# Kernel optimization log

Measured on AMD Instinct MI355X. Metric: run time of the kernel, lower is better.

Reference implementation:

```python
import jax, jax.numpy as jnp
import numpy as np

D_MODEL = 1024
H = 16
D_H = D_MODEL // H
B = 8
S = 1024
NEG_INF = -1e9


def setup_inputs() -> dict:
    key = jax.random.key(0)
    ks = jax.random.split(key, 8)
    Qs = jax.random.normal(ks[0], (B, S, D_MODEL), dtype=jnp.float32)
    Ks = jax.random.normal(ks[1], (B, S, D_MODEL), dtype=jnp.float32)
    Vs = jax.random.normal(ks[2], (B, S, D_MODEL), dtype=jnp.float32)
    mask_3d = jnp.zeros((B, S, S), dtype=bool)
    # Parameters: torch.rand -> uniform[0,1) for per-head projections
    W_Q = jax.random.uniform(ks[3], (H, D_MODEL, D_H), dtype=jnp.float32)
    W_K = jax.random.uniform(ks[4], (H, D_MODEL, D_H), dtype=jnp.float32)
    W_V = jax.random.uniform(ks[5], (H, D_MODEL, D_H), dtype=jnp.float32)
    # Output nn.Linear(h*d_h, d_model): weight [d_model, h*d_h], bias [d_model]
    lim = 1.0 / np.sqrt(H * D_H)
    W_out = jax.random.uniform(ks[6], (D_MODEL, H * D_H), minval=-lim, maxval=lim, dtype=jnp.float32)
    b_out = jax.random.uniform(ks[7], (D_MODEL,), minval=-lim, maxval=lim, dtype=jnp.float32)
    return {"Qs": Qs, "Ks": Ks, "Vs": Vs, "mask_3d": mask_3d,
            "W_Q": W_Q, "W_K": W_K, "W_V": W_V, "W_out": W_out, "b_out": b_out}


def reference(Qs, Ks, Vs, mask_3d, W_Q, W_K, W_V, W_out, b_out):
    # Fused per-head projections: avoid the explicit repeat in the torch code.
    q = jnp.einsum('bsk,hkl->bhsl', Qs, W_Q)  # [B,H,S,D_H]
    k = jnp.einsum('bsk,hkl->bhsl', Ks, W_K)
    v = jnp.einsum('bsk,hkl->bhsl', Vs, W_V)
    scale = 1.0 / jnp.sqrt(jnp.asarray(D_H, dtype=q.dtype))
    scores = jnp.einsum('bhqd,bhkd->bhqk', q, k) * scale  # [B,H,S,S]
    scores = jnp.where(mask_3d[:, None, :, :], NEG_INF, scores)
    attn = jax.nn.softmax(scores, axis=-1)
    out = jnp.einsum('bhqk,bhkd->bhqd', attn, v)  # [B,H,S,D_H]
    # chunk along head-batch dim then cat along feature dim == head-major concat
    out = jnp.transpose(out, (0, 2, 1, 3)).reshape(B, S, H * D_H)
    return out @ W_out.T + b_out
```

## Files before the change

### kernel.cpp

```cpp
#include <hip/hip_runtime.h>

#define DM 1024
#define H_ 16
#define DH 64
#define B_ 8
#define S_ 1024

typedef _Float16 half8 __attribute__((ext_vector_type(8)));
typedef _Float16 half4 __attribute__((ext_vector_type(4)));
typedef __fp16 fp16x2 __attribute__((ext_vector_type(2)));
typedef float f32x4 __attribute__((ext_vector_type(4)));
typedef float f32x16 __attribute__((ext_vector_type(16)));
typedef unsigned int uint;

static __device__ __forceinline__ uint pkrtz(float a, float b) {
    fp16x2 h = __builtin_amdgcn_cvt_pkrtz(a, b);
    return __builtin_bit_cast(uint, h);
}
#define PSWAP(d, s) asm volatile("v_permlane32_swap_b32 %0, %1" : "+v"(d), "+v"(s))

static __device__ __forceinline__ void gload16(const _Float16* g, _Float16* l) {
    __builtin_amdgcn_global_load_lds(
        (const __attribute__((address_space(1))) unsigned int*)(const void*)g,
        (__attribute__((address_space(3))) unsigned int*)(void*)l,
        16, 0, 0);
}

__global__ __launch_bounds__(256) void packw_k(
    const float* __restrict__ WQ, const float* __restrict__ WK,
    const float* __restrict__ WV,
    _Float16* __restrict__ wqh, _Float16* __restrict__ wql,
    _Float16* __restrict__ wkh, _Float16* __restrict__ wkl,
    _Float16* __restrict__ wv)
{
    __shared__ __align__(16) _Float16 Lh[64][72];
    __shared__ __align__(16) _Float16 Ll[64][72];
    const int t = threadIdx.x;
    const int kb = blockIdx.x;
    const int h  = blockIdx.y;

    #pragma unroll
    for (int s = 0; s < 3; ++s) {
        const float* W = (s == 0) ? WQ : ((s == 1) ? WK : WV);
        const int krow = t >> 2, lc = t & 3;
        const float* rp = W + (((size_t)h * 1024 + kb * 64 + krow) * 64 + lc * 16);
        #pragma unroll
        for (int q4 = 0; q4 < 4; ++q4) {
            float4 f = ((const float4*)rp)[q4];
            float vv0 = f.x, vv1 = f.y, vv2 = f.z, vv3 = f.w;
            int l0 = lc * 16 + q4 * 4;
            _Float16 h0 = (_Float16)vv0; Lh[l0 + 0][krow] = h0; Ll[l0 + 0][krow] = (_Float16)(vv0 - (float)h0);
            _Float16 h1 = (_Float16)vv1; Lh[l0 + 1][krow] = h1; Ll[l0 + 1][krow] = (_Float16)(vv1 - (float)h1);
            _Float16 h2 = (_Float16)vv2; Lh[l0 + 2][krow] = h2; Ll[l0 + 2][krow] = (_Float16)(vv2 - (float)h2);
            _Float16 h3 = (_Float16)vv3; Lh[l0 + 3][krow] = h3; Ll[l0 + 3][krow] = (_Float16)(vv3 - (float)h3);
        }
        __syncthreads();
        const int l = t >> 2, pc = t & 3;
        #pragma unroll
        for (int hp = 0; hp < 2; ++hp) {
            int p = pc + 4 * hp;
            int lc2 = p ^ (l & 7);
            half8 vh = *(const half8*)&Lh[l][lc2 * 8];
            half8 vl = *(const half8*)&Ll[l][lc2 * 8];
            size_t off = (size_t)(h * 64 + l) * DM + kb * 64 + p * 8;
            if (s == 0) { *(half8*)(wqh + off) = vh; *(half8*)(wql + off) = vl; }
            else if (s == 1) { *(half8*)(wkh + off) = vh; *(half8*)(wkl + off) = vl; }
            else { *(half8*)(wv + off) = vh; }
        }
        __syncthreads();
    }
}

__global__ __launch_bounds__(256) void packo_k(
    const float* __restrict__ WO, _Float16* __restrict__ wo)
{
    int idx8 = blockIdx.x * 256 + threadIdx.x;
    int n = idx8 >> 7;
    int c = idx8 & 127;
    int p = (c & ~7) | ((c & 7) ^ (n & 7));
    const float* rp = WO + ((size_t)n * DM + c * 8);
    float4 a = ((const float4*)rp)[0];
    float4 b = ((const float4*)rp)[1];
    half8 v;
    v[0] = (_Float16)a.x; v[1] = (_Float16)a.y; v[2] = (_Float16)a.z; v[3] = (_Float16)a.w;
    v[4] = (_Float16)b.x; v[5] = (_Float16)b.y; v[6] = (_Float16)b.z; v[7] = (_Float16)b.w;
    *(half8*)(wo + (size_t)n * DM + p * 8) = v;
}

__global__ __launch_bounds__(256) void scan_k(
    const unsigned char* __restrict__ mask, unsigned char* __restrict__ scan)
{
    __shared__ int s_red[4];
    const int t = threadIdx.x;
    const int q64 = blockIdx.x, k64 = blockIdx.y, b = blockIdx.z;
    uint4 mv = *(const uint4*)(mask + ((size_t)b * S_ + q64 * 64 + (t >> 2)) * S_ + k64 * 64 + (t & 3) * 16);
    int a = (mv.x | mv.y | mv.z | mv.w) != 0;
    unsigned long long bal = __ballot(a);
    if ((t & 63) == 0) s_red[t >> 6] = (bal != 0ull);
    __syncthreads();
    if (t == 0)
        scan[(b * 16 + q64) * 16 + k64] =
            (unsigned char)(s_red[0] | s_red[1] | s_red[2] | s_red[3]);
}

__global__ __launch_bounds__(512) void gemm_split_k(
    const float* __restrict__ A0, const float* __restrict__ A1,
    const _Float16* __restrict__ Bh0, const _Float16* __restrict__ Bl0,
    const _Float16* __restrict__ Bh1, const _Float16* __restrict__ Bl1,
    _Float16* __restrict__ Chi0, _Float16* __restrict__ Clo0,
    _Float16* __restrict__ Chi1, _Float16* __restrict__ Clo1)
{
    const int lid = blockIdx.x + 8 * blockIdx.y + 512 * blockIdx.z;
    const int xcd = lid & 7, k2 = lid >> 3;
    const int G = xcd * 16 + (k2 >> 3);
    const int bxv = k2 & 7, byv = G & 63, z = G >> 6;

    const float* A = z ? A1 : A0;
    const _Float16* Bh = z ? Bh1 : Bh0;
    const _Float16* Bl = z ? Bl1 : Bl0;
    _Float16* Chi = z ? Chi1 : Chi0;
    _Float16* Clo = z ? Clo1 : Clo0;

    __shared__ __align__(16) _Float16 SM[32768];
    _Float16* Ah  = SM;
    _Float16* Al  = SM + 8192;
    _Float16* Bhs = SM + 16384;
    _Float16* Bls = SM + 24576;

    const int t = threadIdx.x;
    const int lane = t & 63;
    const int w = t >> 6;
    const int wm = (w >> 1) * 32;
    const int wn = (w & 1) * 64;
    const int l15 = lane & 15;
    const int l4g = lane >> 4;

    const int bm = byv * 128;
    const int bn = bxv * 128;

    f32x4 acc[2][4] = {};

    float4 ar[4];
    auto aload = [&](int KT) {
        #pragma unroll
        for (int i = 0; i < 4; ++i)
            ar[i] = *(const float4*)(A + (size_t)(bm + (t >> 4) + 32 * i) * DM + KT * 64 + (t & 15) * 4);
    };
    auto awr = [&]() {
        #pragma unroll
        for (int i = 0; i < 4; ++i) {
            int row = (t >> 4) + 32 * i;
            int c4 = t & 15;
            float4 v = ar[i];
            half4 hv, lv;
            hv[0] = (_Float16)v.x; lv[0] = (_Float16)(v.x - (float)hv[0]);
            hv[1] = (_Float16)v.y; lv[1] = (_Float16)(v.y - (float)hv[1]);
            hv[2] = (_Float16)v.z; lv[2] = (_Float16)(v.z - (float)hv[2]);
            hv[3] = (_Float16)v.w; lv[3] = (_Float16)(v.w - (float)hv[3]);
            int off = row * 64 + (((c4 >> 1) ^ (row & 7)) * 8) + (c4 & 1) * 4;
            *(half4*)&Ah[off] = hv;
            *(half4*)&Al[off] = lv;
        }
    };
    auto bgl = [&](int KT) {
        #pragma unroll
        for (int j = 0; j < 2; ++j) {
            int rr = w * 16 + j * 8 + (lane >> 3);
            const size_t so = (size_t)(bn + rr) * DM + KT * 64 + (lane & 7) * 8;
            gload16(Bh + so, &Bhs[(w * 16 + j * 8) * 64]);
            gload16(Bl + so, &Bls[(w * 16 + j * 8) * 64]);
        }
    };

    aload(0);
    bgl(0);
    for (int kt = 0; kt < 16; ++kt) {
        awr();
        __syncthreads();
        if (kt < 15) aload(kt + 1);
        #pragma unroll
        for (int ks = 0; ks < 2; ++ks) {
            half8 ah[2], al[2], bh[4], bl[4];
            const int slotx = (ks * 4 + l4g);
            #pragma unroll
            for (int mi = 0; mi < 2; ++mi) {
                int r = wm + mi * 16 + l15;
                int off = r * 64 + (slotx ^ (l15 & 7)) * 8;
                ah[mi] = *(const half8*)&Ah[off];
                al[mi] = *(const half8*)&Al[off];
            }
            #pragma unroll
            for (int ni = 0; ni < 4; ++ni) {
                int r = wn + ni * 16 + l15;
                int off = r * 64 + (slotx ^ (l15 & 7)) * 8;
                bh[ni] = *(const half8*)&Bhs[off];
                bl[ni] = *(const half8*)&Bls[off];
            }
            #pragma unroll
            for (int mi = 0; mi < 2; ++mi)
                #pragma unroll
                for (int ni = 0; ni < 4; ++ni) {
                    acc[mi][ni] = __builtin_amdgcn_mfma_f32_16x16x32_f16(ah[mi], bh[ni], acc[mi][ni], 0, 0, 0);
                    acc[mi][ni] = __builtin_amdgcn_mfma_f32_16x16x32_f16(ah[mi], bl[ni], acc[mi][ni], 0, 0, 0);
                    acc[mi][ni] = __builtin_amdgcn_mfma_f32_16x16x32_f16(al[mi], bh[ni], acc[mi][ni], 0, 0, 0);
                }
        }
        __syncthreads();
        if (kt < 15) bgl(kt + 1);
    }

    #pragma unroll
    for (int mi = 0; mi < 2; ++mi)
        #pragma unroll
        for (int ni = 0; ni < 4; ++ni) {
            int col = bn + wn + ni * 16 + l15;
            #pragma unroll
            for (int r = 0; r < 4; ++r) {
                int row = bm + wm + mi * 16 + l4g * 4 + r;
                float val = acc[mi][ni][r];
                _Float16 hv = (_Float16)val;
                Chi[(size_t)row * DM + col] = hv;
                Clo[(size_t)row * DM + col] = (_Float16)(val - (float)hv);
            }
        }
}

__global__ __launch_bounds__(256) void gemm_v_k(
    const float* __restrict__ A, const _Float16* __restrict__ Bt,
    _Float16* __restrict__ C)
{
    const int lid = blockIdx.x + 8 * blockIdx.y;
    const int xcd = lid & 7, k2 = lid >> 3;
    const int G = xcd * 8 + (k2 >> 3);
    const int bxv = k2 & 7, byv = G;

    __shared__ __align__(16) _Float16 SM[25600];
    _Float16* As  = SM;
    _Float16* Bsb = SM + 9216;

    const int t = threadIdx.x;
    const int lane = t & 63;
    const int w = t >> 6;
    const int wm = (w >> 1) * 64;
    const int wn = (w & 1) * 64;
    const int l15 = lane & 15;
    const int l4g = lane >> 4;

    const int bm = byv * 128;
    const int bn = bxv * 128;

    f32x4 acc[4][4] = {};

    const int arow = t >> 4, ac4 = t & 15;
    float4 ar[8];
    auto aload = [&](int KT) {
        #pragma unroll
        for (int i = 0; i < 8; ++i)
            ar[i] = *(const float4*)(A + (size_t)(bm + arow + 16 * i) * DM + KT * 64 + ac4 * 4);
    };
    auto awr = [&]() {
        #pragma unroll
        for (int i = 0; i < 8; ++i) {
            float4 v = ar[i];
            half4 hv;
            hv[0] = (_Float16)v.x; hv[1] = (_Float16)v.y;
            hv[2] = (_Float16)v.z; hv[3] = (_Float16)v.w;
            *(half4*)&As[(arow + 16 * i) * 72 + ac4 * 4] = hv;
        }
    };
    auto bgl = [&](int KT, int buf) {
        _Float16* Bd = Bsb + buf * 8192;
        #pragma unroll
        for (int j = 0; j < 4; ++j) {
            int rr = w * 32 + j * 8 + (lane >> 3);
            gload16(Bt + (size_t)(bn + rr) * DM + KT * 64 + (lane & 7) * 8,
                    &Bd[(w * 32 + j * 8) * 64]);
        }
    };

    aload(0);
    bgl(0, 0);
    for (int kt = 0; kt < 16; ++kt) {
        const _Float16* Bcur = Bsb + (kt & 1) * 8192;
        awr();
        __syncthreads();
        if (kt < 15) { aload(kt + 1); bgl(kt + 1, (kt + 1) & 1); }
        #pragma unroll
        for (int ks = 0; ks < 2; ++ks) {
            half8 a[4], b[4];
            #pragma unroll
            for (int mi = 0; mi < 4; ++mi)
                a[mi] = *(const half8*)&As[(wm + mi * 16 + l15) * 72 + ks * 32 + l4g * 8];
            #pragma unroll
            for (int ni = 0; ni < 4; ++ni) {
                int row = wn + ni * 16 + l15;
                int slot = (ks * 4 + l4g) ^ (l15 & 7);
                b[ni] = *(const half8*)&Bcur[row * 64 + slot * 8];
            }
            #pragma unroll
            for (int mi = 0; mi < 4; ++mi)
                #pragma unroll
                for (int ni = 0; ni < 4; ++ni)
                    acc[mi][ni] = __builtin_amdgcn_mfma_f32_16x16x32_f16(a[mi], b[ni], acc[mi][ni], 0, 0, 0);
        }
        __syncthreads();
    }

    _Float16* Tw = SM + w * 4608;
    #pragma unroll
    for (int mi = 0; mi < 4; ++mi)
        #pragma unroll
        for (int ni = 0; ni < 4; ++ni)
            #pragma unroll
            for (int r = 0; r < 4; ++r)
                Tw[(ni * 16 + l15) * 72 + mi * 16 + l4g * 4 + r] = (_Float16)acc[mi][ni][r];
    __syncthreads();
    {
        const int mg0 = bm + wm;
        const int b = mg0 >> 10, s0 = mg0 & 1023;
        _Float16* op = C + ((size_t)b * DM + (bn + wn + lane)) * S_ + s0;
        #pragma unroll
        for (int c8 = 0; c8 < 8; ++c8)
            *(half8*)(op + c8 * 8) = *(const half8*)&Tw[lane * 72 + c8 * 8];
    }
}

__global__ __launch_bounds__(256) void gemm_out_k(
    const _Float16* __restrict__ A, const _Float16* __restrict__ Bt,
    float* __restrict__ C, const float* __restrict__ bias)
{
    const int lid = blockIdx.x + 8 * blockIdx.y;
    const int xcd = lid & 7, k2 = lid >> 3;
    const int G = xcd * 8 + (k2 >> 3);
    const int bxv = k2 & 7, byv = G;

    __shared__ __align__(16) _Float16 SM[25600];
    _Float16* As  = SM;
    _Float16* Bsb = SM + 9216;

    const int t = threadIdx.x;
    const int lane = t & 63;
    const int w = t >> 6;
    const int wm = (w >> 1) * 64;
    const int wn = (w & 1) * 64;
    const int l15 = lane & 15;
    const int l4g = lane >> 4;

    const int bm = byv * 128;
    const int bn = bxv * 128;

    f32x4 acc[4][4] = {};

    uint4 arr[4];
    auto aload = [&](int KT) {
        #pragma unroll
        for (int i = 0; i < 4; ++i)
            arr[i] = *(const uint4*)(A + (size_t)(bm + (t >> 3) + 32 * i) * DM + KT * 64 + (t & 7) * 8);
    };
    auto awr = [&]() {
        #pragma unroll
        for (int i = 0; i < 4; ++i)
            *(uint4*)&As[((t >> 3) + 32 * i) * 72 + (t & 7) * 8] = arr[i];
    };
    auto bgl = [&](int KT, int buf) {
        _Float16* Bd = Bsb + buf * 8192;
        #pragma unroll
        for (int j = 0; j < 4; ++j) {
            int rr = w * 32 + j * 8 + (lane >> 3);
            gload16(Bt + (size_t)(bn + rr) * DM + KT * 64 + (lane & 7) * 8,
                    &Bd[(w * 32 + j * 8) * 64]);
        }
    };

    aload(0);
    bgl(0, 0);
    for (int kt = 0; kt < 16; ++kt) {
        const _Float16* Bcur = Bsb + (kt & 1) * 8192;
        awr();
        __syncthreads();
        if (kt < 15) { aload(kt + 1); bgl(kt + 1, (kt + 1) & 1); }
        #pragma unroll
        for (int ks = 0; ks < 2; ++ks) {
            half8 a[4], b[4];
            #pragma unroll
            for (int mi = 0; mi < 4; ++mi)
                a[mi] = *(const half8*)&As[(wm + mi * 16 + l15) * 72 + ks * 32 + l4g * 8];
            #pragma unroll
            for (int ni = 0; ni < 4; ++ni) {
                int row = wn + ni * 16 + l15;
                int slot = (ks * 4 + l4g) ^ (l15 & 7);
                b[ni] = *(const half8*)&Bcur[row * 64 + slot * 8];
            }
            #pragma unroll
            for (int mi = 0; mi < 4; ++mi)
                #pragma unroll
                for (int ni = 0; ni < 4; ++ni)
                    acc[mi][ni] = __builtin_amdgcn_mfma_f32_16x16x32_f16(a[mi], b[ni], acc[mi][ni], 0, 0, 0);
        }
        __syncthreads();
    }

    #pragma unroll
    for (int mi = 0; mi < 4; ++mi)
        #pragma unroll
        for (int ni = 0; ni < 4; ++ni) {
            int col = bn + wn + ni * 16 + l15;
            #pragma unroll
            for (int r = 0; r < 4; ++r) {
                int row = bm + wm + mi * 16 + l4g * 4 + r;
                C[(size_t)row * DM + col] = acc[mi][ni][r] + bias[col];
            }
        }
}

__global__ __launch_bounds__(256) void attn_k(
    const _Float16* __restrict__ qhg, const _Float16* __restrict__ qlg,
    const _Float16* __restrict__ khg, const _Float16* __restrict__ klg,
    const _Float16* __restrict__ vtg, const unsigned char* __restrict__ maskg,
    const unsigned char* __restrict__ scanp, _Float16* __restrict__ ho)
{
    __shared__ __align__(16) _Float16 Kh[64][72];
    __shared__ __align__(16) _Float16 Kl[64][72];
    __shared__ __align__(16) _Float16 Vt[64][72];

    const int t = threadIdx.x;
    const int lane = t & 63;
    const int w = t >> 6;
    const int l31 = lane & 31;
    const int hi = lane >> 5;

    const int j = blockIdx.y + 16 * blockIdx.z;
    const int head = 16 * blockIdx.x + (j >> 3);
    const int qt = j & 7;
    const int h = head & 15;
    const int b = head >> 4;

    const int colbase = h * DH;
    const int qrow = qt * 128 + w * 32 + l31;

    half8 qfh[4], qfl[4];
    {
        const size_t base = ((size_t)b * S_ + qrow) * DM + colbase;
        #pragma unroll
        for (int ds = 0; ds < 4; ++ds) {
            qfh[ds] = *(const half8*)(qhg + base + ds * 16 + hi * 8);
            qfl[ds] = *(const half8*)(qlg + base + ds * 16 + hi * 8);
        }
    }

    float m_q = -1e30f, ls = 0.0f;
    f32x16 accO0 = {};
    f32x16 accO1 = {};

    const int r0 = t >> 3;
    const int c0 = (t & 7) * 8;
    const _Float16* kph = khg + ((size_t)b * S_) * DM + colbase;
    const _Float16* kpl = klg + ((size_t)b * S_) * DM + colbase;
    const _Float16* vp  = vtg + ((size_t)b * DM + colbase) * S_;
    const unsigned char* sc0 = scanp + (b * 16 + 2 * qt) * 16;
    const unsigned char* sc1 = scanp + (b * 16 + 2 * qt + 1) * 16;

    uint4 akh0, akh1, akl0, akl1, av0, av1;
#define ALOAD(KT) do { \
        akh0 = *(const uint4*)(kph + (size_t)((KT) * 64 + r0) * DM + c0);       \
        akh1 = *(const uint4*)(kph + (size_t)((KT) * 64 + 32 + r0) * DM + c0);  \
        akl0 = *(const uint4*)(kpl + (size_t)((KT) * 64 + r0) * DM + c0);       \
        akl1 = *(const uint4*)(kpl + (size_t)((KT) * 64 + 32 + r0) * DM + c0);  \
        av0  = *(const uint4*)(vp + (size_t)r0 * S_ + (KT) * 64 + c0);          \
        av1  = *(const uint4*)(vp + (size_t)(32 + r0) * S_ + (KT) * 64 + c0);   \
    } while (0)
#define AWRITE() do { \
        *(uint4*)&Kh[r0][c0] = akh0; *(uint4*)&Kh[32 + r0][c0] = akh1; \
        *(uint4*)&Kl[r0][c0] = akl0; *(uint4*)&Kl[32 + r0][c0] = akl1; \
        *(uint4*)&Vt[r0][c0] = av0;  *(uint4*)&Vt[32 + r0][c0] = av1;  \
    } while (0)

    ALOAD(0);
    AWRITE();
    int msk = sc0[0] | sc1[0];

    const float SC = 0.125f * 1.44269504089f;
    const float THRRAW = 8.0f / SC;

    for (int kt = 0; kt < 16; ++kt) {
        __syncthreads();
        const int mskcur = msk;
        if (kt < 15) {
            ALOAD(kt + 1);
            msk = sc0[kt + 1] | sc1[kt + 1];
        }

        f32x16 sa0 = {}, sa1 = {};
        __builtin_amdgcn_s_setprio(1);
        #pragma unroll
        for (int ds = 0; ds < 4; ++ds) {
            half8 kh0 = *(const half8*)&Kh[l31][ds * 16 + hi * 8];
            half8 kl0 = *(const half8*)&Kl[l31][ds * 16 + hi * 8];
            half8 kh1 = *(const half8*)&Kh[32 + l31][ds * 16 + hi * 8];
            half8 kl1 = *(const half8*)&Kl[32 + l31][ds * 16 + hi * 8];
            sa0 = __builtin_amdgcn_mfma_f32_32x32x16_f16(kh0, qfh[ds], sa0, 0, 0, 0);
            sa0 = __builtin_amdgcn_mfma_f32_32x32x16_f16(kh0, qfl[ds], sa0, 0, 0, 0);
            sa0 = __builtin_amdgcn_mfma_f32_32x32x16_f16(kl0, qfh[ds], sa0, 0, 0, 0);
            sa1 = __builtin_amdgcn_mfma_f32_32x32x16_f16(kh1, qfh[ds], sa1, 0, 0, 0);
            sa1 = __builtin_amdgcn_mfma_f32_32x32x16_f16(kh1, qfl[ds], sa1, 0, 0, 0);
            sa1 = __builtin_amdgcn_mfma_f32_32x32x16_f16(kl1, qfh[ds], sa1, 0, 0, 0);
        }
        __builtin_amdgcn_s_setprio(0);

        if (mskcur) {
            const unsigned char* mrow = maskg + ((size_t)b * S_ + qrow) * S_ + kt * 64;
            #pragma unroll
            for (int e = 0; e < 16; ++e) {
                int kl_ = (e & 3) + 8 * (e >> 2) + 4 * hi;
                if (mrow[kl_]) sa0[e] = -1e9f;
                if (mrow[32 + kl_]) sa1[e] = -1e9f;
            }
        }

        float rm = sa0[0];
        #pragma unroll
        for (int e = 1; e < 16; ++e) rm = fmaxf(rm, sa0[e]);
        #pragma unroll
        for (int e = 0; e < 16; ++e) rm = fmaxf(rm, sa1[e]);
        rm = fmaxf(rm, __shfl_xor(rm, 32));
        if (__any(rm > m_q + THRRAW)) {
            const float mn = fmaxf(m_q, rm);
            const float sfac = exp2f((m_q - mn) * SC);
            m_q = mn;
            ls *= sfac;
            #pragma unroll
            for (int e = 0; e < 16; ++e) { accO0[e] *= sfac; accO1[e] *= sfac; }
        }
        const float nmn = -m_q * SC;
        float rs = 0.0f;
        #pragma unroll
        for (int e = 0; e < 16; ++e) { sa0[e] = exp2f(fmaf(sa0[e], SC, nmn)); rs += sa0[e]; }
        #pragma unroll
        for (int e = 0; e < 16; ++e) { sa1[e] = exp2f(fmaf(sa1[e], SC, nmn)); rs += sa1[e]; }
        rs += __shfl_xor(rs, 32);
        ls += rs;

        half8 pf[4];
        {
            uint c0_ = pkrtz(sa0[0], sa0[1]),  c1_ = pkrtz(sa0[2], sa0[3]);
            uint c2_ = pkrtz(sa0[4], sa0[5]),  c3_ = pkrtz(sa0[6], sa0[7]);
            uint c4_ = pkrtz(sa0[8], sa0[9]),  c5_ = pkrtz(sa0[10], sa0[11]);
            uint c6_ = pkrtz(sa0[12], sa0[13]), c7_ = pkrtz(sa0[14], sa0[15]);
            PSWAP(c0_, c2_); PSWAP(c1_, c3_);
            PSWAP(c4_, c6_); PSWAP(c5_, c7_);
            uint4 u0 = {c0_, c1_, c2_, c3_}, u1 = {c4_, c5_, c6_, c7_};
            pf[0] = __builtin_bit_cast(half8, u0);
            pf[1] = __builtin_bit_cast(half8, u1);
        }
        {
            uint c0_ = pkrtz(sa1[0], sa1[1]),  c1_ = pkrtz(sa1[2], sa1[3]);
            uint c2_ = pkrtz(sa1[4], sa1[5]),  c3_ = pkrtz(sa1[6], sa1[7]);
            uint c4_ = pkrtz(sa1[8], sa1[9]),  c5_ = pkrtz(sa1[10], sa1[11]);
            uint c6_ = pkrtz(sa1[12], sa1[13]), c7_ = pkrtz(sa1[14], sa1[15]);
            PSWAP(c0_, c2_); PSWAP(c1_, c3_);
            PSWAP(c4_, c6_); PSWAP(c5_, c7_);
            uint4 u0 = {c0_, c1_, c2_, c3_}, u1 = {c4_, c5_, c6_, c7_};
            pf[2] = __builtin_bit_cast(half8, u0);
            pf[3] = __builtin_bit_cast(half8, u1);
        }
        __builtin_amdgcn_s_setprio(1);
        #pragma unroll
        for (int kc = 0; kc < 4; ++kc) {
            half8 vf0 = *(const half8*)&Vt[l31][kc * 16 + hi * 8];
            half8 vf1 = *(const half8*)&Vt[32 + l31][kc * 16 + hi * 8];
            accO0 = __builtin_amdgcn_mfma_f32_32x32x16_f16(vf0, pf[kc], accO0, 0, 0, 0);
            accO1 = __builtin_amdgcn_mfma_f32_32x32x16_f16(vf1, pf[kc], accO1, 0, 0, 0);
        }
        __builtin_amdgcn_s_setprio(0);

        __syncthreads();
        if (kt < 15) AWRITE();
    }
#undef ALOAD
#undef AWRITE

    const float inv = 1.0f / ls;
    _Float16* orow = ho + ((size_t)b * S_ + qrow) * DM + colbase;
    #pragma unroll
    for (int g2 = 0; g2 < 4; ++g2) {
        half4 hv0, hv1;
        #pragma unroll
        for (int e = 0; e < 4; ++e) {
            hv0[e] = (_Float16)(accO0[g2 * 4 + e] * inv);
            hv1[e] = (_Float16)(accO1[g2 * 4 + e] * inv);
        }
        *(half4*)(orow + g2 * 8 + hi * 4) = hv0;
        *(half4*)(orow + 32 + g2 * 8 + hi * 4) = hv1;
    }
}

extern "C" void kernel_launch(void* const* d_in, const int* in_sizes, int n_in,
                              void* d_out, int out_size, void* d_ws, size_t ws_size,
                              hipStream_t stream)
{
    const float* Qs = (const float*)d_in[0];
    const float* Ks = (const float*)d_in[1];
    const float* Vs = (const float*)d_in[2];
    const unsigned char* mask = (const unsigned char*)d_in[3];
    const float* WQ = (const float*)d_in[4];
    const float* WK = (const float*)d_in[5];
    const float* WV = (const float*)d_in[6];
    const float* WO = (const float*)d_in[7];
    const float* bo = (const float*)d_in[8];

    char* ws = (char*)d_ws;
    const size_t MB = 1024 * 1024;
    _Float16* wqh = (_Float16*)(ws + 0 * MB);
    _Float16* wql = (_Float16*)(ws + 2 * MB);
    _Float16* wkh = (_Float16*)(ws + 4 * MB);
    _Float16* wkl = (_Float16*)(ws + 6 * MB);
    _Float16* wv  = (_Float16*)(ws + 8 * MB);
    _Float16* wo  = (_Float16*)(ws + 10 * MB);
    _Float16* qhi = (_Float16*)(ws + 12 * MB);
    _Float16* qlo = (_Float16*)(ws + 28 * MB);
    _Float16* khi = (_Float16*)(ws + 44 * MB);
    _Float16* klo = (_Float16*)(ws + 60 * MB);
    _Float16* vt  = (_Float16*)(ws + 76 * MB);
    _Float16* hh  = (_Float16*)(ws + 92 * MB);
    unsigned char* scan = (unsigned char*)(ws + 108 * MB);

    packw_k<<<dim3(16, 16), 256, 0, stream>>>(WQ, WK, WV, wqh, wql, wkh, wkl, wv);
    packo_k<<<512, 256, 0, stream>>>(WO, wo);
    scan_k<<<dim3(16, 16, 8), 256, 0, stream>>>(mask, scan);

    gemm_split_k<<<dim3(8, 64, 2), 512, 0, stream>>>(
        Qs, Ks, wqh, wql, wkh, wkl, qhi, qlo, khi, klo);

    gemm_v_k<<<dim3(8, 64), 256, 0, stream>>>(Vs, wv, vt);

    attn_k<<<dim3(8, 16, 8), 256, 0, stream>>>(qhi, qlo, khi, klo, vt, mask, scan, hh);

    gemm_out_k<<<dim3(8, 64), 256, 0, stream>>>(hh, wo, (float*)d_out, bo);
}
```

Measured before the change: 305.7 us.

## Load GEMM A operands directly into MFMA registers and double-buffer B tiles

In the three projection and output GEMMs, the A operand is now read straight from global memory into registers in MFMA fragment layout. This drops the LDS staging step, the fp16 split done at LDS-write time, and one barrier per k-step. The B tile becomes double-buffered in LDS so the next tile's async load overlaps the current MFMAs. gemm_v and gemm_out move to 512 threads with smaller per-wave tiles. The cost is uncoalesced per-lane A reads (32-byte chunks per row) and more register pressure for the prefetched fp32 fragments.

Result: slower. 374.9 us (+22.6%).

```diff
diff --git a/kernel.cpp b/kernel.cpp
--- a/kernel.cpp
+++ b/kernel.cpp
@@ -24,6 +24,17 @@
         (const __attribute__((address_space(1))) unsigned int*)(const void*)g,
         (__attribute__((address_space(3))) unsigned int*)(void*)l,
         16, 0, 0);
+}
+
+static __device__ __forceinline__ void cvt8(float4 a, float4 b, half8& hv, half8& lv) {
+    hv[0] = (_Float16)a.x; lv[0] = (_Float16)(a.x - (float)hv[0]);
+    hv[1] = (_Float16)a.y; lv[1] = (_Float16)(a.y - (float)hv[1]);
+    hv[2] = (_Float16)a.z; lv[2] = (_Float16)(a.z - (float)hv[2]);
+    hv[3] = (_Float16)a.w; lv[3] = (_Float16)(a.w - (float)hv[3]);
+    hv[4] = (_Float16)b.x; lv[4] = (_Float16)(b.x - (float)hv[4]);
+    hv[5] = (_Float16)b.y; lv[5] = (_Float16)(b.y - (float)hv[5]);
+    hv[6] = (_Float16)b.z; lv[6] = (_Float16)(b.z - (float)hv[6]);
+    hv[7] = (_Float16)b.w; lv[7] = (_Float16)(b.w - (float)hv[7]);
 }
 
 __global__ __launch_bounds__(256) void packw_k(
@@ -122,10 +133,6 @@
     _Float16* Clo = z ? Clo1 : Clo0;
 
     __shared__ __align__(16) _Float16 SM[32768];
-    _Float16* Ah  = SM;
-    _Float16* Al  = SM + 8192;
-    _Float16* Bhs = SM + 16384;
-    _Float16* Bls = SM + 24576;
 
     const int t = threadIdx.x;
     const int lane = t & 63;
@@ -140,73 +147,62 @@
 
     f32x4 acc[2][4] = {};
 
-    float4 ar[4];
+    const float* aptr = A + (size_t)(bm + wm + l15) * DM + l4g * 8;
+    float4 arf[8];
     auto aload = [&](int KT) {
         #pragma unroll
-        for (int i = 0; i < 4; ++i)
-            ar[i] = *(const float4*)(A + (size_t)(bm + (t >> 4) + 32 * i) * DM + KT * 64 + (t & 15) * 4);
-    };
-    auto awr = [&]() {
-        #pragma unroll
-        for (int i = 0; i < 4; ++i) {
-            int row = (t >> 4) + 32 * i;
-            int c4 = t & 15;
-            float4 v = ar[i];
-            half4 hv, lv;
-            hv[0] = (_Float16)v.x; lv[0] = (_Float16)(v.x - (float)hv[0]);
-            hv[1] = (_Float16)v.y; lv[1] = (_Float16)(v.y - (float)hv[1]);
-            hv[2] = (_Float16)v.z; lv[2] = (_Float16)(v.z - (float)hv[2]);
-            hv[3] = (_Float16)v.w; lv[3] = (_Float16)(v.w - (float)hv[3]);
-            int off = row * 64 + (((c4 >> 1) ^ (row & 7)) * 8) + (c4 & 1) * 4;
-            *(half4*)&Ah[off] = hv;
-            *(half4*)&Al[off] = lv;
-        }
-    };
-    auto bgl = [&](int KT) {
-        #pragma unroll
-        for (int j = 0; j < 2; ++j) {
-            int rr = w * 16 + j * 8 + (lane >> 3);
+        for (int mi = 0; mi < 2; ++mi)
+            #pragma unroll
+            for (int ks = 0; ks < 2; ++ks) {
+                const float* p = aptr + (size_t)mi * 16 * DM + KT * 64 + ks * 32;
+                arf[(mi * 2 + ks) * 2 + 0] = *(const float4*)p;
+                arf[(mi * 2 + ks) * 2 + 1] = *(const float4*)(p + 4);
+            }
+    };
+    half8 ahf[4], alf[4];
+    auto acvt = [&]() {
+        #pragma unroll
+        for (int f = 0; f < 4; ++f)
+            cvt8(arf[f * 2], arf[f * 2 + 1], ahf[f], alf[f]);
+    };
+    auto bgl = [&](int KT, int buf) {
+        _Float16* Bhd = SM + buf * 16384;
+        _Float16* Bld = Bhd + 8192;
+        #pragma unroll
+        for (int jj = 0; jj < 2; ++jj) {
+            int rr = w * 16 + jj * 8 + (lane >> 3);
             const size_t so = (size_t)(bn + rr) * DM + KT * 64 + (lane & 7) * 8;
-            gload16(Bh + so, &Bhs[(w * 16 + j * 8) * 64]);
-            gload16(Bl + so, &Bls[(w * 16 + j * 8) * 64]);
+            gload16(Bh + so, Bhd + (w * 16 + jj * 8) * 64);
+            gload16(Bl + so, Bld + (w * 16 + jj * 8) * 64);
         }
     };
 
     aload(0);
-    bgl(0);
+    bgl(0, 0);
+    __syncthreads();
     for (int kt = 0; kt < 16; ++kt) {
-        awr();
+        acvt();
+        if (kt < 15) { aload(kt + 1); bgl(kt + 1, (kt + 1) & 1); }
+        const _Float16* Bhc = SM + (kt & 1) * 16384;
+        const _Float16* Blc = Bhc + 8192;
+        #pragma unroll
+        for (int ks = 0; ks < 2; ++ks) {
+            const int slotx = ks * 4 + l4g;
+            #pragma unroll
+            for (int ni = 0; ni < 4; ++ni) {
+                int off = (wn + ni * 16 + l15) * 64 + ((slotx ^ (l15 & 7)) * 8);
+                half8 bh = *(const half8*)&Bhc[off];
+                half8 bl = *(const half8*)&Blc[off];
+                #pragma unroll
+                for (int mi = 0; mi < 2; ++mi) {
+                    const int f = mi * 2 + ks;
+                    acc[mi][ni] = __builtin_amdgcn_mfma_f32_16x16x32_f16(ahf[f], bh, acc[mi][ni], 0, 0, 0);
+                    acc[mi][ni] = __builtin_amdgcn_mfma_f32_16x16x32_f16(ahf[f], bl, acc[mi][ni], 0, 0, 0);
+                    acc[mi][ni] = __builtin_amdgcn_mfma_f32_16x16x32_f16(alf[f], bh, acc[mi][ni], 0, 0, 0);
+                }
+            }
+        }
         __syncthreads();
-        if (kt < 15) aload(kt + 1);
-        #pragma unroll
-        for (int ks = 0; ks < 2; ++ks) {
-            half8 ah[2], al[2], bh[4], bl[4];
-            const int slotx = (ks * 4 + l4g);
-            #pragma unroll
-            for (int mi = 0; mi < 2; ++mi) {
-                int r = wm + mi * 16 + l15;
-                int off = r * 64 + (slotx ^ (l15 & 7)) * 8;
-                ah[mi] = *(const half8*)&Ah[off];
-                al[mi] = *(const half8*)&Al[off];
-            }
-            #pragma unroll
-            for (int ni = 0; ni < 4; ++ni) {
-                int r = wn + ni * 16 + l15;
-                int off = r * 64 + (slotx ^ (l15 & 7)) * 8;
-                bh[ni] = *(const half8*)&Bhs[off];
-                bl[ni] = *(const half8*)&Bls[off];
-            }
-            #pragma unroll
-            for (int mi = 0; mi < 2; ++mi)
-                #pragma unroll
-                for (int ni = 0; ni < 4; ++ni) {
-                    acc[mi][ni] = __builtin_amdgcn_mfma_f32_16x16x32_f16(ah[mi], bh[ni], acc[mi][ni], 0, 0, 0);
-                    acc[mi][ni] = __builtin_amdgcn_mfma_f32_16x16x32_f16(ah[mi], bl[ni], acc[mi][ni], 0, 0, 0);
-                    acc[mi][ni] = __builtin_amdgcn_mfma_f32_16x16x32_f16(al[mi], bh[ni], acc[mi][ni], 0, 0, 0);
-                }
-        }
-        __syncthreads();
-        if (kt < 15) bgl(kt + 1);
     }
 
     #pragma unroll
@@ -225,7 +221,7 @@
         }
 }
 
-__global__ __launch_bounds__(256) void gemm_v_k(
+__global__ __launch_bounds__(512) void gemm_v_k(
     const float* __restrict__ A, const _Float16* __restrict__ Bt,
     _Float16* __restrict__ C)
 {
@@ -234,14 +230,12 @@
     const int G = xcd * 8 + (k2 >> 3);
     const int bxv = k2 & 7, byv = G;
 
-    __shared__ __align__(16) _Float16 SM[25600];
-    _Float16* As  = SM;
-    _Float16* Bsb = SM + 9216;
+    __shared__ __align__(16) _Float16 SM[18432];
 
     const int t = threadIdx.x;
     const int lane = t & 63;
     const int w = t >> 6;
-    const int wm = (w >> 1) * 64;
+    const int wm = (w >> 1) * 32;
     const int wn = (w & 1) * 64;
     const int l15 = lane & 15;
     const int l4g = lane >> 4;
@@ -249,83 +243,84 @@
     const int bm = byv * 128;
     const int bn = bxv * 128;
 
-    f32x4 acc[4][4] = {};
-
-    const int arow = t >> 4, ac4 = t & 15;
-    float4 ar[8];
+    f32x4 acc[2][4] = {};
+
+    const float* aptr = A + (size_t)(bm + wm + l15) * DM + l4g * 8;
+    float4 arf[8];
     auto aload = [&](int KT) {
         #pragma unroll
-        for (int i = 0; i < 8; ++i)
-            ar[i] = *(const float4*)(A + (size_t)(bm + arow + 16 * i) * DM + KT * 64 + ac4 * 4);
-    };
-    auto awr = [&]() {
-        #pragma unroll
-        for (int i = 0; i < 8; ++i) {
-            float4 v = ar[i];
-            half4 hv;
-            hv[0] = (_Float16)v.x; hv[1] = (_Float16)v.y;
-            hv[2] = (_Float16)v.z; hv[3] = (_Float16)v.w;
-            *(half4*)&As[(arow + 16 * i) * 72 + ac4 * 4] = hv;
+        for (int mi = 0; mi < 2; ++mi)
+            #pragma unroll
+            for (int ks = 0; ks < 2; ++ks) {
+                const float* p = aptr + (size_t)mi * 16 * DM + KT * 64 + ks * 32;
+                arf[(mi * 2 + ks) * 2 + 0] = *(const float4*)p;
+                arf[(mi * 2 + ks) * 2 + 1] = *(const float4*)(p + 4);
+            }
+    };
+    half8 ahf[4];
+    auto acvt = [&]() {
+        #pragma unroll
+        for (int f = 0; f < 4; ++f) {
+            float4 a = arf[f * 2], b = arf[f * 2 + 1];
+            half8 hv;
+            hv[0] = (_Float16)a.x; hv[1] = (_Float16)a.y;
+            hv[2] = (_Float16)a.z; hv[3] = (_Float16)a.w;
+            hv[4] = (_Float16)b.x; hv[5] = (_Float16)b.y;
+            hv[6] = (_Float16)b.z; hv[7] = (_Float16)b.w;
+            ahf[f] = hv;
         }
     };
     auto bgl = [&](int KT, int buf) {
-        _Float16* Bd = Bsb + buf * 8192;
-        #pragma unroll
-        for (int j = 0; j < 4; ++j) {
-            int rr = w * 32 + j * 8 + (lane >> 3);
+        _Float16* Bd = SM + buf * 8192;
+        #pragma unroll
+        for (int jj = 0; jj < 2; ++jj) {
+            int rr = w * 16 + jj * 8 + (lane >> 3);
             gload16(Bt + (size_t)(bn + rr) * DM + KT * 64 + (lane & 7) * 8,
-                    &Bd[(w * 32 + j * 8) * 64]);
+                    Bd + (w * 16 + jj * 8) * 64);
         }
     };
 
     aload(0);
     bgl(0, 0);
+    __syncthreads();
     for (int kt = 0; kt < 16; ++kt) {
-        const _Float16* Bcur = Bsb + (kt & 1) * 8192;
-        awr();
+        acvt();
+        if (kt < 15) { aload(kt + 1); bgl(kt + 1, (kt + 1) & 1); }
+        const _Float16* Bc = SM + (kt & 1) * 8192;
+        #pragma unroll
+        for (int ks = 0; ks < 2; ++ks) {
+            const int slotx = ks * 4 + l4g;
+            #pragma unroll
+            for (int ni = 0; ni < 4; ++ni) {
+                int off = (wn + ni * 16 + l15) * 64 + ((slotx ^ (l15 & 7)) * 8);
+                half8 b = *(const half8*)&Bc[off];
+                #pragma unroll
+                for (int mi = 0; mi < 2; ++mi)
+                    acc[mi][ni] = __builtin_amdgcn_mfma_f32_16x16x32_f16(ahf[mi * 2 + ks], b, acc[mi][ni], 0, 0, 0);
+            }
+        }
         __syncthreads();
-        if (kt < 15) { aload(kt + 1); bgl(kt + 1, (kt + 1) & 1); }
-        #pragma unroll
-        for (int ks = 0; ks < 2; ++ks) {
-            half8 a[4], b[4];
-            #pragma unroll
-            for (int mi = 0; mi < 4; ++mi)
-                a[mi] = *(const half8*)&As[(wm + mi * 16 + l15) * 72 + ks * 32 + l4g * 8];
-            #pragma unroll
-            for (int ni = 0; ni < 4; ++ni) {
-                int row = wn + ni * 16 + l15;
-                int slot = (ks * 4 + l4g) ^ (l15 & 7);
-                b[ni] = *(const half8*)&Bcur[row * 64 + slot * 8];
-            }
-            #pragma unroll
-            for (int mi = 0; mi < 4; ++mi)
-                #pragma unroll
-                for (int ni = 0; ni < 4; ++ni)
-                    acc[mi][ni] = __builtin_amdgcn_mfma_f32_16x16x32_f16(a[mi], b[ni], acc[mi][ni], 0, 0, 0);
-        }
-        __syncthreads();
-    }
-
-    _Float16* Tw = SM + w * 4608;
+    }
+
+    _Float16* Tw = SM + w * 2304;
     #pragma unroll
-    for (int mi = 0; mi < 4; ++mi)
+    for (int mi = 0; mi < 2; ++mi)
         #pragma unroll
         for (int ni = 0; ni < 4; ++ni)
             #pragma unroll
             for (int r = 0; r < 4; ++r)
-                Tw[(ni * 16 + l15) * 72 + mi * 16 + l4g * 4 + r] = (_Float16)acc[mi][ni][r];
-    __syncthreads();
+                Tw[(ni * 16 + l15) * 36 + mi * 16 + l4g * 4 + r] = (_Float16)acc[mi][ni][r];
     {
         const int mg0 = bm + wm;
-        const int b = mg0 >> 10, s0 = mg0 & 1023;
-        _Float16* op = C + ((size_t)b * DM + (bn + wn + lane)) * S_ + s0;
-        #pragma unroll
-        for (int c8 = 0; c8 < 8; ++c8)
-            *(half8*)(op + c8 * 8) = *(const half8*)&Tw[lane * 72 + c8 * 8];
-    }
-}
-
-__global__ __launch_bounds__(256) void gemm_out_k(
+        const int bb = mg0 >> 10, s0 = mg0 & 1023;
+        _Float16* op = C + ((size_t)bb * DM + (bn + wn + lane)) * S_ + s0;
+        #pragma unroll
+        for (int c8 = 0; c8 < 4; ++c8)
+            *(half8*)(op + c8 * 8) = *(const half8*)&Tw[lane * 36 + c8 * 8];
+    }
+}
+
+__global__ __launch_bounds__(512) void gemm_out_k(
     const _Float16* __restrict__ A, const _Float16* __restrict__ Bt,
     float* __restrict__ C, const float* __restrict__ bias)
 {
@@ -334,14 +329,12 @@
     const int G = xcd * 8 + (k2 >> 3);
     const int bxv = k2 & 7, byv = G;
 
-    __shared__ __align__(16) _Float16 SM[25600];
-    _Float16* As  = SM;
-    _Float16* Bsb = SM + 9216;
+    __shared__ __align__(16) _Float16 SM[16384];
 
     const int t = threadIdx.x;
     const int lane = t & 63;
     const int w = t >> 6;
-    const int wm = (w >> 1) * 64;
+    const int wm = (w >> 1) * 32;
     const int wn = (w & 1) * 64;
     const int l15 = lane & 15;
     const int l4g = lane >> 4;
@@ -349,59 +342,55 @@
     const int bm = byv * 128;
     const int bn = bxv * 128;
 
-    f32x4 acc[4][4] = {};
-
-    uint4 arr[4];
-    auto aload = [&](int KT) {
-        #pragma unroll
-        for (int i = 0; i < 4; ++i)
-            arr[i] = *(const uint4*)(A + (size_t)(bm + (t >> 3) + 32 * i) * DM + KT * 64 + (t & 7) * 8);
-    };
-    auto awr = [&]() {
-        #pragma unroll
-        for (int i = 0; i < 4; ++i)
-            *(uint4*)&As[((t >> 3) + 32 * i) * 72 + (t & 7) * 8] = arr[i];
+    f32x4 acc[2][4] = {};
+
+    const _Float16* aptr = A + (size_t)(bm + wm + l15) * DM + l4g * 8;
+    auto aloadTo = [&](half8 (&dst)[4], int KT) {
+        #pragma unroll
+        for (int mi = 0; mi < 2; ++mi)
+            #pragma unroll
+            for (int ks = 0; ks < 2; ++ks)
+                dst[mi * 2 + ks] = *(const half8*)(aptr + (size_t)mi * 16 * DM + KT * 64 + ks * 32);
     };
     auto bgl = [&](int KT, int buf) {
-        _Float16* Bd = Bsb + buf * 8192;
-        #pragma unroll
-        for (int j = 0; j < 4; ++j) {
-            int rr = w * 32 + j * 8 + (lane >> 3);
+        _Float16* Bd = SM + buf * 8192;
+        #pragma unroll
+        for (int jj = 0; jj < 2; ++jj) {
+            int rr = w * 16 + jj * 8 + (lane >> 3);
             gload16(Bt + (size_t)(bn + rr) * DM + KT * 64 + (lane & 7) * 8,
-                    &Bd[(w * 32 + j * 8) * 64]);
-        }
-    };
-
-    aload(0);
+                    Bd + (w * 16 + jj * 8) * 64);
+        }
+    };
+    auto body = [&](half8 (&cur)[4], half8 (&nxt)[4], int kt) {
+        if (kt < 15) { aloadTo(nxt, kt + 1); bgl(kt + 1, (kt + 1) & 1); }
+        const _Float16* Bc = SM + (kt & 1) * 8192;
+        #pragma unroll
+        for (int ks = 0; ks < 2; ++ks) {
+            const int slotx = ks * 4 + l4g;
+            #pragma unroll
+            for (int ni = 0; ni < 4; ++ni) {
+                int off = (wn + ni * 16 + l15) * 64 + ((slotx ^ (l15 & 7)) * 8);
+                half8 b = *(const half8*)&Bc[off];
+                #pragma unroll
+                for (int mi = 0; mi < 2; ++mi)
+                    acc[mi][ni] = __builtin_amdgcn_mfma_f32_16x16x32_f16(cur[mi * 2 + ks], b, acc[mi][ni], 0, 0, 0);
+            }
+        }
+        __syncthreads();
+    };
+
+    half8 afA[4], afB[4];
+    aloadTo(afA, 0);
     bgl(0, 0);
-    for (int kt = 0; kt < 16; ++kt) {
-        const _Float16* Bcur = Bsb + (kt & 1) * 8192;
-        awr();
-        __syncthreads();
-        if (kt < 15) { aload(kt + 1); bgl(kt + 1, (kt + 1) & 1); }
-        #pragma unroll
-        for (int ks = 0; ks < 2; ++ks) {
-            half8 a[4], b[4];
-            #pragma unroll
-            for (int mi = 0; mi < 4; ++mi)
-                a[mi] = *(const half8*)&As[(wm + mi * 16 + l15) * 72 + ks * 32 + l4g * 8];
-            #pragma unroll
-            for (int ni = 0; ni < 4; ++ni) {
-                int row = wn + ni * 16 + l15;
-                int slot = (ks * 4 + l4g) ^ (l15 & 7);
-                b[ni] = *(const half8*)&Bcur[row * 64 + slot * 8];
-            }
-            #pragma unroll
-            for (int mi = 0; mi < 4; ++mi)
-                #pragma unroll
-                for (int ni = 0; ni < 4; ++ni)
-                    acc[mi][ni] = __builtin_amdgcn_mfma_f32_16x16x32_f16(a[mi], b[ni], acc[mi][ni], 0, 0, 0);
-        }
-        __syncthreads();
-    }
-
+    __syncthreads();
     #pragma unroll
-    for (int mi = 0; mi < 4; ++mi)
+    for (int k8 = 0; k8 < 8; ++k8) {
+        body(afA, afB, 2 * k8);
+        body(afB, afA, 2 * k8 + 1);
+    }
+
+    #pragma unroll
+    for (int mi = 0; mi < 2; ++mi)
         #pragma unroll
         for (int ni = 0; ni < 4; ++ni) {
             int col = bn + wn + ni * 16 + l15;
@@ -631,9 +620,9 @@
     gemm_split_k<<<dim3(8, 64, 2), 512, 0, stream>>>(
         Qs, Ks, wqh, wql, wkh, wkl, qhi, qlo, khi, klo);
 
-    gemm_v_k<<<dim3(8, 64), 256, 0, stream>>>(Vs, wv, vt);
+    gemm_v_k<<<dim3(8, 64), 512, 0, stream>>>(Vs, wv, vt);
 
     attn_k<<<dim3(8, 16, 8), 256, 0, stream>>>(qhi, qlo, khi, klo, vt, mask, scan, hh);
 
-    gemm_out_k<<<dim3(8, 64), 256, 0, stream>>>(hh, wo, (float*)d_out, bo);
-}
+    gemm_out_k<<<dim3(8, 64), 512, 0, stream>>>(hh, wo, (float*)d_out, bo);
+}
```

## Double-buffer split-fp16 projection GEMM with 32-wide K tiles and new swizzle

Applied to the files above, without the earlier changes.

Restructures the Q/K projection GEMM to use double-buffered LDS with K-tiles of 32 instead of 64, prefetching the next A and B tiles while computing the current one. This needs only one barrier per iteration instead of two. The weight packing kernel changes its swizzle for Q/K to match the new 32-column B layout, and A uses padded rows (stride 40) in place of an XOR swizzle. It is meant to overlap global loads with MFMA work. The cost is twice as many loop iterations and more shared memory, which may lower occupancy.

Result: slower. 315.1 us (+3.1%).

```diff
diff --git a/kernel.cpp b/kernel.cpp
--- a/kernel.cpp
+++ b/kernel.cpp
@@ -24,6 +24,17 @@
         (const __attribute__((address_space(1))) unsigned int*)(const void*)g,
         (__attribute__((address_space(3))) unsigned int*)(void*)l,
         16, 0, 0);
+}
+
+static __device__ __forceinline__ void cvt8(float4 a, float4 b, half8& hv, half8& lv) {
+    hv[0] = (_Float16)a.x; lv[0] = (_Float16)(a.x - (float)hv[0]);
+    hv[1] = (_Float16)a.y; lv[1] = (_Float16)(a.y - (float)hv[1]);
+    hv[2] = (_Float16)a.z; lv[2] = (_Float16)(a.z - (float)hv[2]);
+    hv[3] = (_Float16)a.w; lv[3] = (_Float16)(a.w - (float)hv[3]);
+    hv[4] = (_Float16)b.x; lv[4] = (_Float16)(b.x - (float)hv[4]);
+    hv[5] = (_Float16)b.y; lv[5] = (_Float16)(b.y - (float)hv[5]);
+    hv[6] = (_Float16)b.z; lv[6] = (_Float16)(b.z - (float)hv[6]);
+    hv[7] = (_Float16)b.w; lv[7] = (_Float16)(b.w - (float)hv[7]);
 }
 
 __global__ __launch_bounds__(256) void packw_k(
@@ -59,7 +70,8 @@
         #pragma unroll
         for (int hp = 0; hp < 2; ++hp) {
             int p = pc + 4 * hp;
-            int lc2 = p ^ (l & 7);
+            int lc2 = (s == 2) ? (p ^ (l & 7))
+                               : ((p & 4) | ((p & 3) ^ ((l >> 2) & 3)));
             half8 vh = *(const half8*)&Lh[l][lc2 * 8];
             half8 vl = *(const half8*)&Ll[l][lc2 * 8];
             size_t off = (size_t)(h * 64 + l) * DM + kb * 64 + p * 8;
@@ -105,8 +117,8 @@
 
 __global__ __launch_bounds__(512) void gemm_split_k(
     const float* __restrict__ A0, const float* __restrict__ A1,
-    const _Float16* __restrict__ Bh0, const _Float16* __restrict__ Bl0,
-    const _Float16* __restrict__ Bh1, const _Float16* __restrict__ Bl1,
+    const _Float16* __restrict__ Bhg0, const _Float16* __restrict__ Blg0,
+    const _Float16* __restrict__ Bhg1, const _Float16* __restrict__ Blg1,
     _Float16* __restrict__ Chi0, _Float16* __restrict__ Clo0,
     _Float16* __restrict__ Chi1, _Float16* __restrict__ Clo1)
 {
@@ -116,16 +128,12 @@
     const int bxv = k2 & 7, byv = G & 63, z = G >> 6;
 
     const float* A = z ? A1 : A0;
-    const _Float16* Bh = z ? Bh1 : Bh0;
-    const _Float16* Bl = z ? Bl1 : Bl0;
+    const _Float16* Bhg = z ? Bhg1 : Bhg0;
+    const _Float16* Blg = z ? Blg1 : Blg0;
     _Float16* Chi = z ? Chi1 : Chi0;
     _Float16* Clo = z ? Clo1 : Clo0;
 
-    __shared__ __align__(16) _Float16 SM[32768];
-    _Float16* Ah  = SM;
-    _Float16* Al  = SM + 8192;
-    _Float16* Bhs = SM + 16384;
-    _Float16* Bls = SM + 24576;
+    __shared__ __align__(16) _Float16 SM[36864];
 
     const int t = threadIdx.x;
     const int lane = t & 63;
@@ -140,73 +148,54 @@
 
     f32x4 acc[2][4] = {};
 
-    float4 ar[4];
+    const int arow = t >> 2, ac = t & 3;
+    const float* ap = A + (size_t)(bm + arow) * DM + ac * 8;
+    float4 ar0, ar1;
     auto aload = [&](int KT) {
-        #pragma unroll
-        for (int i = 0; i < 4; ++i)
-            ar[i] = *(const float4*)(A + (size_t)(bm + (t >> 4) + 32 * i) * DM + KT * 64 + (t & 15) * 4);
-    };
-    auto awr = [&]() {
-        #pragma unroll
-        for (int i = 0; i < 4; ++i) {
-            int row = (t >> 4) + 32 * i;
-            int c4 = t & 15;
-            float4 v = ar[i];
-            half4 hv, lv;
-            hv[0] = (_Float16)v.x; lv[0] = (_Float16)(v.x - (float)hv[0]);
-            hv[1] = (_Float16)v.y; lv[1] = (_Float16)(v.y - (float)hv[1]);
-            hv[2] = (_Float16)v.z; lv[2] = (_Float16)(v.z - (float)hv[2]);
-            hv[3] = (_Float16)v.w; lv[3] = (_Float16)(v.w - (float)hv[3]);
-            int off = row * 64 + (((c4 >> 1) ^ (row & 7)) * 8) + (c4 & 1) * 4;
-            *(half4*)&Ah[off] = hv;
-            *(half4*)&Al[off] = lv;
-        }
-    };
-    auto bgl = [&](int KT) {
-        #pragma unroll
-        for (int j = 0; j < 2; ++j) {
-            int rr = w * 16 + j * 8 + (lane >> 3);
-            const size_t so = (size_t)(bn + rr) * DM + KT * 64 + (lane & 7) * 8;
-            gload16(Bh + so, &Bhs[(w * 16 + j * 8) * 64]);
-            gload16(Bl + so, &Bls[(w * 16 + j * 8) * 64]);
-        }
-    };
-
-    aload(0);
-    bgl(0);
-    for (int kt = 0; kt < 16; ++kt) {
-        awr();
-        __syncthreads();
-        if (kt < 15) aload(kt + 1);
-        #pragma unroll
-        for (int ks = 0; ks < 2; ++ks) {
-            half8 ah[2], al[2], bh[4], bl[4];
-            const int slotx = (ks * 4 + l4g);
-            #pragma unroll
-            for (int mi = 0; mi < 2; ++mi) {
-                int r = wm + mi * 16 + l15;
-                int off = r * 64 + (slotx ^ (l15 & 7)) * 8;
-                ah[mi] = *(const half8*)&Ah[off];
-                al[mi] = *(const half8*)&Al[off];
+        ar0 = *(const float4*)(ap + KT * 32);
+        ar1 = *(const float4*)(ap + KT * 32 + 4);
+    };
+    auto awr = [&](int buf) {
+        half8 hv, lv;
+        cvt8(ar0, ar1, hv, lv);
+        *(half8*)&SM[buf * 5120 + arow * 40 + ac * 8] = hv;
+        *(half8*)&SM[10240 + buf * 5120 + arow * 40 + ac * 8] = lv;
+    };
+    const size_t bso = (size_t)(bn + arow) * DM + ac * 8;
+    auto bgl = [&](int KT, int buf) {
+        gload16(Bhg + bso + KT * 32, &SM[20480 + buf * 4096 + w * 512]);
+        gload16(Blg + bso + KT * 32, &SM[28672 + buf * 4096 + w * 512]);
+    };
+
+    aload(0); bgl(0, 0); awr(0);
+    __syncthreads();
+    for (int kt = 0; kt < 32; ++kt) {
+        const int buf = kt & 1;
+        if (kt < 31) { aload(kt + 1); bgl(kt + 1, buf ^ 1); }
+        half8 bh[4], bl[4], ah[2], al[2];
+        #pragma unroll
+        for (int ni = 0; ni < 4; ++ni) {
+            int row = wn + ni * 16 + l15;
+            int p8 = l4g ^ ((row >> 2) & 3);
+            bh[ni] = *(const half8*)&SM[20480 + buf * 4096 + row * 32 + p8 * 8];
+            bl[ni] = *(const half8*)&SM[28672 + buf * 4096 + row * 32 + p8 * 8];
+        }
+        #pragma unroll
+        for (int mi = 0; mi < 2; ++mi) {
+            int row = wm + mi * 16 + l15;
+            ah[mi] = *(const half8*)&SM[buf * 5120 + row * 40 + l4g * 8];
+            al[mi] = *(const half8*)&SM[10240 + buf * 5120 + row * 40 + l4g * 8];
+        }
+        #pragma unroll
+        for (int mi = 0; mi < 2; ++mi)
+            #pragma unroll
+            for (int ni = 0; ni < 4; ++ni) {
+                acc[mi][ni] = __builtin_amdgcn_mfma_f32_16x16x32_f16(ah[mi], bh[ni], acc[mi][ni], 0, 0, 0);
+                acc[mi][ni] = __builtin_amdgcn_mfma_f32_16x16x32_f16(ah[mi], bl[ni], acc[mi][ni], 0, 0, 0);
+                acc[mi][ni] = __builtin_amdgcn_mfma_f32_16x16x32_f16(al[mi], bh[ni], acc[mi][ni], 0, 0, 0);
             }
-            #pragma unroll
-            for (int ni = 0; ni < 4; ++ni) {
-                int r = wn + ni * 16 + l15;
-                int off = r * 64 + (slotx ^ (l15 & 7)) * 8;
-                bh[ni] = *(const half8*)&Bhs[off];
-                bl[ni] = *(const half8*)&Bls[off];
-            }
-            #pragma unroll
-            for (int mi = 0; mi < 2; ++mi)
-                #pragma unroll
-                for (int ni = 0; ni < 4; ++ni) {
-                    acc[mi][ni] = __builtin_amdgcn_mfma_f32_16x16x32_f16(ah[mi], bh[ni], acc[mi][ni], 0, 0, 0);
-                    acc[mi][ni] = __builtin_amdgcn_mfma_f32_16x16x32_f16(ah[mi], bl[ni], acc[mi][ni], 0, 0, 0);
-                    acc[mi][ni] = __builtin_amdgcn_mfma_f32_16x16x32_f16(al[mi], bh[ni], acc[mi][ni], 0, 0, 0);
-                }
-        }
-        __syncthreads();
-        if (kt < 15) bgl(kt + 1);
+        if (kt < 31) awr(buf ^ 1);
+        __syncthreads();
     }
 
     #pragma unroll
```

## Double attention block to 512 threads covering 256 query rows per tile

Applied to the files above, without the earlier changes.

The attention kernel now runs 8 waves per block, each handling 32 query rows, so each block covers 256 queries instead of 128 and the grid is halved. Each K/V tile loaded into shared memory is reused by twice as many queries, and each thread loads one chunk per tile instead of two, which cuts global K/V traffic per query. The mask scan now ORs four 64-row groups. The trade-off is fewer blocks in flight and heavier barriers across eight waves, and register limits under the 512 launch bound may be tighter. The renaming of loop variables in the GEMM kernels is cosmetic.

New measurement: 309.0 us. Within noise of the previous version (+1.1%).

```diff
diff --git a/kernel.cpp b/kernel.cpp
--- a/kernel.cpp
+++ b/kernel.cpp
@@ -164,11 +164,11 @@
     };
     auto bgl = [&](int KT) {
         #pragma unroll
-        for (int j = 0; j < 2; ++j) {
-            int rr = w * 16 + j * 8 + (lane >> 3);
+        for (int jj = 0; jj < 2; ++jj) {
+            int rr = w * 16 + jj * 8 + (lane >> 3);
             const size_t so = (size_t)(bn + rr) * DM + KT * 64 + (lane & 7) * 8;
-            gload16(Bh + so, &Bhs[(w * 16 + j * 8) * 64]);
-            gload16(Bl + so, &Bls[(w * 16 + j * 8) * 64]);
+            gload16(Bh + so, &Bhs[(w * 16 + jj * 8) * 64]);
+            gload16(Bl + so, &Bls[(w * 16 + jj * 8) * 64]);
         }
     };
 
@@ -271,10 +271,10 @@
     auto bgl = [&](int KT, int buf) {
         _Float16* Bd = Bsb + buf * 8192;
         #pragma unroll
-        for (int j = 0; j < 4; ++j) {
-            int rr = w * 32 + j * 8 + (lane >> 3);
+        for (int jj = 0; jj < 4; ++jj) {
+            int rr = w * 32 + jj * 8 + (lane >> 3);
             gload16(Bt + (size_t)(bn + rr) * DM + KT * 64 + (lane & 7) * 8,
-                    &Bd[(w * 32 + j * 8) * 64]);
+                    &Bd[(w * 32 + jj * 8) * 64]);
         }
     };
 
@@ -365,10 +365,10 @@
     auto bgl = [&](int KT, int buf) {
         _Float16* Bd = Bsb + buf * 8192;
         #pragma unroll
-        for (int j = 0; j < 4; ++j) {
-            int rr = w * 32 + j * 8 + (lane >> 3);
+        for (int jj = 0; jj < 4; ++jj) {
+            int rr = w * 32 + jj * 8 + (lane >> 3);
             gload16(Bt + (size_t)(bn + rr) * DM + KT * 64 + (lane & 7) * 8,
-                    &Bd[(w * 32 + j * 8) * 64]);
+                    &Bd[(w * 32 + jj * 8) * 64]);
         }
     };
 
@@ -413,7 +413,7 @@
         }
 }
 
-__global__ __launch_bounds__(256) void attn_k(
+__global__ __launch_bounds__(512) void attn_k(
     const _Float16* __restrict__ qhg, const _Float16* __restrict__ qlg,
     const _Float16* __restrict__ khg, const _Float16* __restrict__ klg,
     const _Float16* __restrict__ vtg, const unsigned char* __restrict__ maskg,
@@ -429,14 +429,14 @@
     const int l31 = lane & 31;
     const int hi = lane >> 5;
 
-    const int j = blockIdx.y + 16 * blockIdx.z;
-    const int head = 16 * blockIdx.x + (j >> 3);
-    const int qt = j & 7;
+    const int j = blockIdx.y + 8 * blockIdx.z;
+    const int head = 16 * blockIdx.x + (j >> 2);
+    const int qt = j & 3;
     const int h = head & 15;
     const int b = head >> 4;
 
     const int colbase = h * DH;
-    const int qrow = qt * 128 + w * 32 + l31;
+    const int qrow = qt * 256 + w * 32 + l31;
 
     half8 qfh[4], qfl[4];
     {
@@ -457,27 +457,24 @@
     const _Float16* kph = khg + ((size_t)b * S_) * DM + colbase;
     const _Float16* kpl = klg + ((size_t)b * S_) * DM + colbase;
     const _Float16* vp  = vtg + ((size_t)b * DM + colbase) * S_;
-    const unsigned char* sc0 = scanp + (b * 16 + 2 * qt) * 16;
-    const unsigned char* sc1 = scanp + (b * 16 + 2 * qt + 1) * 16;
-
-    uint4 akh0, akh1, akl0, akl1, av0, av1;
+    const unsigned char* scb = scanp + (b * 16 + 4 * qt) * 16;
+
+    uint4 akh, akl, av;
 #define ALOAD(KT) do { \
-        akh0 = *(const uint4*)(kph + (size_t)((KT) * 64 + r0) * DM + c0);       \
-        akh1 = *(const uint4*)(kph + (size_t)((KT) * 64 + 32 + r0) * DM + c0);  \
-        akl0 = *(const uint4*)(kpl + (size_t)((KT) * 64 + r0) * DM + c0);       \
-        akl1 = *(const uint4*)(kpl + (size_t)((KT) * 64 + 32 + r0) * DM + c0);  \
-        av0  = *(const uint4*)(vp + (size_t)r0 * S_ + (KT) * 64 + c0);          \
-        av1  = *(const uint4*)(vp + (size_t)(32 + r0) * S_ + (KT) * 64 + c0);   \
+        akh = *(const uint4*)(kph + (size_t)((KT) * 64 + r0) * DM + c0);   \
+        akl = *(const uint4*)(kpl + (size_t)((KT) * 64 + r0) * DM + c0);   \
+        av  = *(const uint4*)(vp + (size_t)r0 * S_ + (KT) * 64 + c0);      \
     } while (0)
 #define AWRITE() do { \
-        *(uint4*)&Kh[r0][c0] = akh0; *(uint4*)&Kh[32 + r0][c0] = akh1; \
-        *(uint4*)&Kl[r0][c0] = akl0; *(uint4*)&Kl[32 + r0][c0] = akl1; \
-        *(uint4*)&Vt[r0][c0] = av0;  *(uint4*)&Vt[32 + r0][c0] = av1;  \
+        *(uint4*)&Kh[r0][c0] = akh; \
+        *(uint4*)&Kl[r0][c0] = akl; \
+        *(uint4*)&Vt[r0][c0] = av;  \
     } while (0)
+#define SCAN(KT) (scb[KT] | scb[16 + (KT)] | scb[32 + (KT)] | scb[48 + (KT)])
 
     ALOAD(0);
     AWRITE();
-    int msk = sc0[0] | sc1[0];
+    int msk = SCAN(0);
 
     const float SC = 0.125f * 1.44269504089f;
     const float THRRAW = 8.0f / SC;
@@ -487,7 +484,7 @@
         const int mskcur = msk;
         if (kt < 15) {
             ALOAD(kt + 1);
-            msk = sc0[kt + 1] | sc1[kt + 1];
+            msk = SCAN(kt + 1);
         }
 
         f32x16 sa0 = {}, sa1 = {};
@@ -578,6 +575,7 @@
     }
 #undef ALOAD
 #undef AWRITE
+#undef SCAN
 
     const float inv = 1.0f / ls;
     _Float16* orow = ho + ((size_t)b * S_ + qrow) * DM + colbase;
@@ -633,7 +631,7 @@
 
     gemm_v_k<<<dim3(8, 64), 256, 0, stream>>>(Vs, wv, vt);
 
-    attn_k<<<dim3(8, 16, 8), 256, 0, stream>>>(qhi, qlo, khi, klo, vt, mask, scan, hh);
+    attn_k<<<dim3(8, 8, 8), 512, 0, stream>>>(qhi, qlo, khi, klo, vt, mask, scan, hh);
 
     gemm_out_k<<<dim3(8, 64), 256, 0, stream>>>(hh, wo, (float*)d_out, bo);
 }
```
